# Performance work log

Hardware: AMD Instinct MI355X
Metric: run time of the kernel (lower is better)

The kernel has to match this reference:

```python
import jax, jax.numpy as jnp
import numpy as np

B, N, D = 8, 4096, 256

def setup_inputs() -> dict:
    key = jax.random.key(0)
    k1, k2, k3 = jax.random.split(key, 3)
    x = jax.random.normal(k1, (B, N, D), dtype=jnp.float32)
    # torch nn.Linear(D, 3D): weight [3D, D], bias [3D]
    W_qkv = jax.random.normal(k2, (3 * D, D), dtype=jnp.float32) * (1.0 / np.sqrt(D))
    b_qkv = jax.random.normal(k3, (3 * D,), dtype=jnp.float32) * 0.01
    return {"x": x, "W_qkv": W_qkv, "b_qkv": b_qkv}

def reference(x, W_qkv, b_qkv):
    Dm = x.shape[-1]
    qkv = jnp.einsum('bnd,ed->bne', x, W_qkv) + b_qkv  # [B,N,3D]
    q, k, v = jnp.split(qkv, 3, axis=-1)
    scale = 1.0 / jnp.sqrt(jnp.asarray(Dm, dtype=x.dtype))
    scores = jnp.einsum('bnd,bmd->bnm', q, k) * scale  # [B,N,N]
    attn = jax.nn.softmax(scores, axis=-1)
    return jnp.einsum('bnm,bmd->bnd', attn, v)
```

## Files before the change

### kernel.cpp

```cpp
#include <hip/hip_runtime.h>
#include <hip/hip_bf16.h>


typedef __attribute__((ext_vector_type(8))) short short8;
typedef __attribute__((ext_vector_type(4))) float f32x4;
typedef __attribute__((ext_vector_type(16))) float f32x16;

#define MFMA16(A, B, C) __builtin_amdgcn_mfma_f32_16x16x32_bf16(A, B, C, 0, 0, 0)
#define MFMA32(A, B, C) __builtin_amdgcn_mfma_f32_32x32x16_bf16(A, B, C, 0, 0, 0)

__device__ __forceinline__ unsigned short f2bf(float f) {
  union { float f; unsigned u; } v; v.f = f;
  unsigned r = v.u + 0x7FFFu + ((v.u >> 16) & 1u);
  return (unsigned short)(r >> 16);
}

__device__ __forceinline__ ushort4 pack4(float4 v) {
  ushort4 r;
  r.x = f2bf(v.x); r.y = f2bf(v.y); r.z = f2bf(v.z); r.w = f2bf(v.w);
  return r;
}

__device__ __forceinline__ unsigned packbf2(float a, float b) {
  union { __hip_bfloat162 b2; unsigned u; } cv;
  cv.b2 = __float22bfloat162_rn(make_float2(a, b));
  return cv.u;
}

__device__ __forceinline__ void gload_lds16(const void* g, void* l) {
  __builtin_amdgcn_global_load_lds(
      (const __attribute__((address_space(1))) void*)g,
      (__attribute__((address_space(3))) void*)l, 16, 0, 0);
}

template <int MODE>
__global__ __launch_bounds__(256)
void proj_kernel(const float* __restrict__ A, const float* __restrict__ Bm,
                 const float* __restrict__ bias,
                 unsigned short* __restrict__ Qs, unsigned short* __restrict__ Kb,
                 unsigned short* __restrict__ VT) {
  __shared__ __align__(16) unsigned short as_[2][128 * 64];
  __shared__ __align__(16) unsigned short bs_[2][128 * 64];

  const int tid = threadIdx.x;
  const int wid = tid >> 6, lane = tid & 63, l15 = lane & 15, lhi = lane >> 4;
  int m0, n0;
  if (MODE == 0) { m0 = blockIdx.y * 128; n0 = blockIdx.x * 128; }
  else           { m0 = blockIdx.x * 128; n0 = blockIdx.y * 128; }
  const float* Arow = A + (size_t)m0 * 256;
  const float* Brow = Bm + (size_t)n0 * 256;

  const int srow = tid >> 4;
  const int c4 = tid & 15;
  float4 ra[8], rb[8];

  auto loadslice = [&](int kc) {
#pragma unroll
    for (int i = 0; i < 8; ++i) {
      int row = i * 16 + srow;
      ra[i] = *(const float4*)(Arow + (size_t)row * 256 + kc * 64 + c4 * 4);
      rb[i] = *(const float4*)(Brow + (size_t)row * 256 + kc * 64 + c4 * 4);
    }
  };
  auto writeslice = [&](int buf) {
#pragma unroll
    for (int i = 0; i < 8; ++i) {
      int row = i * 16 + srow;
      int g = c4 >> 1, half = c4 & 1;
      int off = row * 64 + ((g ^ (row & 7)) << 3) + half * 4;
      *(ushort4*)&as_[buf][off] = pack4(ra[i]);
      *(ushort4*)&bs_[buf][off] = pack4(rb[i]);
    }
  };

  f32x4 acc[2][8];
#pragma unroll
  for (int mt = 0; mt < 2; ++mt)
#pragma unroll
    for (int nt = 0; nt < 8; ++nt) acc[mt][nt] = (f32x4){0.f, 0.f, 0.f, 0.f};

  loadslice(0);
  writeslice(0);
  int cur = 0;
  for (int kc = 0; kc < 4; ++kc) {
    __syncthreads();
    if (kc < 3) loadslice(kc + 1);
#pragma unroll
    for (int ks = 0; ks < 2; ++ks) {
      short8 af[2];
#pragma unroll
      for (int mt = 0; mt < 2; ++mt) {
        int row = wid * 32 + mt * 16 + l15;
        int g = ks * 4 + lhi;
        af[mt] = *(const short8*)&as_[cur][row * 64 + ((g ^ (row & 7)) << 3)];
      }
#pragma unroll
      for (int nt = 0; nt < 8; ++nt) {
        int row = nt * 16 + l15;
        int g = ks * 4 + lhi;
        short8 bf = *(const short8*)&bs_[cur][row * 64 + ((g ^ (row & 7)) << 3)];
        acc[0][nt] = MFMA16(af[0], bf, acc[0][nt]);
        acc[1][nt] = MFMA16(af[1], bf, acc[1][nt]);
      }
    }
    if (kc < 3) writeslice(cur ^ 1);
    cur ^= 1;
  }

  const float QSC = 0.0901684400555602f;
#pragma unroll
  for (int nt = 0; nt < 8; ++nt) {
    if (MODE == 0) {
      int e = n0 + nt * 16 + l15;
      float bv = bias[e];
#pragma unroll
      for (int mt = 0; mt < 2; ++mt)
#pragma unroll
        for (int r = 0; r < 4; ++r) {
          int tok = m0 + wid * 32 + mt * 16 + lhi * 4 + r;
          float val = acc[mt][nt][r] + bv;
          if (e < 256) Qs[(size_t)tok * 256 + e] = f2bf(val * QSC);
          else         Kb[(size_t)tok * 256 + (e - 256)] = f2bf(val);
        }
    } else {
      int tok = n0 + nt * 16 + l15;
      int bb = tok >> 12, n = tok & 4095;
      int t4 = n & 15;
      int flip = ((t4 >> 2) ^ (t4 >> 3)) & 1;
      int n2 = (n & ~15) | (t4 ^ (flip ? 12 : 0));
#pragma unroll
      for (int mt = 0; mt < 2; ++mt)
#pragma unroll
        for (int r = 0; r < 4; ++r) {
          int d = m0 + wid * 32 + mt * 16 + lhi * 4 + r;
          float val = acc[mt][nt][r] + bias[512 + d];
          VT[(size_t)bb * (256 * 4096) + (size_t)d * 4096 + n2] = f2bf(val);
        }
    }
  }
}

__global__ __launch_bounds__(256, 2)
void attn_split(const unsigned short* __restrict__ Qs,
                const unsigned short* __restrict__ Kb,
                const unsigned short* __restrict__ VT,
                float* __restrict__ out, float* __restrict__ O1,
                float2* __restrict__ ML) {
  __shared__ __align__(16) unsigned short lds_kv[2][16384];

  const int tid = threadIdx.x;
  const int wid = tid >> 6, lane = tid & 63, l31 = lane & 31, h = lane >> 5;
  const int blk = blockIdx.x;
  const int b = blk & 7;
  const int hh = (blk >> 3) & 1;
  const int qblk = blk >> 4;
  const int q0 = qblk * 128 + wid * 32;

  const unsigned short* qp = Qs + ((size_t)b * 4096 + q0 + l31) * 256 + h * 8;
  short8 qf[16];
#pragma unroll
  for (int ks = 0; ks < 16; ++ks) qf[ks] = *(const short8*)(qp + ks * 16);

  f32x16 acco[8];
#pragma unroll
  for (int dt = 0; dt < 8; ++dt)
#pragma unroll
    for (int j = 0; j < 16; ++j) acco[dt][j] = 0.f;
  float m = -1e30f, lsum = 0.f;

  const unsigned short* kbase = Kb + (size_t)b * 4096 * 256;
  const unsigned short* vtb   = VT + (size_t)b * 256 * 4096;

  auto stage = [&](int it, int buf) {
    const int kv0 = hh * 2048 + it * 32;
    unsigned short* kbuf = &lds_kv[buf][0];
    unsigned short* vbuf = &lds_kv[buf][8192];
    const unsigned short* ksrc = kbase + (size_t)kv0 * 256;
#pragma unroll
    for (int i = 0; i < 4; ++i) {
      int g = i * 256 + tid;
      int row = g >> 5, cp = g & 31;
      int sg = (row << 5) | (cp ^ (row & 7));
      gload_lds16(ksrc + sg * 8, kbuf + (i * 256 + (wid << 6)) * 8);
    }
#pragma unroll
    for (int i = 0; i < 4; ++i) {
      int g = i * 256 + tid;
      int d = g >> 2, cp = g & 3;
      int sc = cp ^ ((d >> 1) & 3);
      gload_lds16(vtb + (size_t)d * 4096 + kv0 + sc * 8,
                  vbuf + (i * 256 + (wid << 6)) * 8);
    }
  };

  stage(0, 0);
  int cur = 0;
  for (int it = 0; it < 64; ++it) {
    __syncthreads();
    if (it < 63) stage(it + 1, cur ^ 1);
    const unsigned short* kb = &lds_kv[cur][0];
    const unsigned short* vb = &lds_kv[cur][8192];

    f32x16 s0;
#pragma unroll
    for (int j = 0; j < 16; ++j) s0[j] = 0.f;
    __builtin_amdgcn_s_setprio(1);
#pragma unroll
    for (int ks = 0; ks < 16; ++ks) {
      const short8 kf =
          *(const short8*)&kb[l31 * 256 + (((2 * ks + h) ^ (l31 & 7)) << 3)];
      s0 = MFMA32(kf, qf[ks], s0);
    }
    __builtin_amdgcn_s_setprio(0);

    float mx = s0[0];
#pragma unroll
    for (int r = 1; r < 16; ++r) mx = fmaxf(mx, s0[r]);
    mx = fmaxf(mx, __shfl_xor(mx, 32));
    const float mo = m;
    const float mn = (mx > mo + 4.f) ? mx : mo;
    const float al = __builtin_amdgcn_exp2f(mo - mn);
    m = mn;
    if (__any(mn != mo)) {
      float alq[16];
#pragma unroll
      for (int r = 0; r < 16; ++r)
        alq[r] = __shfl(al, (r & 3) + 8 * (r >> 2) + 4 * h, 64);
#pragma unroll
      for (int dt = 0; dt < 8; ++dt)
#pragma unroll
        for (int r = 0; r < 16; ++r) acco[dt][r] *= alq[r];
    }

#pragma unroll
    for (int r = 0; r < 8; ++r) s0[r] = __builtin_amdgcn_exp2f(s0[r] - mn);
    short8 pf0;
    {
      union { unsigned u[4]; short8 v; } a0;
#pragma unroll
      for (int k2 = 0; k2 < 4; ++k2)
        a0.u[k2] = packbf2(s0[2 * k2], s0[2 * k2 + 1]);
      pf0 = a0.v;
    }
    __builtin_amdgcn_s_setprio(1);
#pragma unroll
    for (int dt = 0; dt < 8; ++dt) {
      const int d = dt * 32 + l31;
      const short8 vf =
          *(const short8*)&vb[d * 32 + ((h ^ ((l31 >> 1) & 3)) << 3)];
      acco[dt] = MFMA32(pf0, vf, acco[dt]);
    }
    __builtin_amdgcn_s_setprio(0);
#pragma unroll
    for (int r = 8; r < 16; ++r) s0[r] = __builtin_amdgcn_exp2f(s0[r] - mn);
    short8 pf1;
    {
      union { unsigned u[4]; short8 v; } a1;
#pragma unroll
      for (int k2 = 0; k2 < 4; ++k2)
        a1.u[k2] = packbf2(s0[8 + 2 * k2], s0[9 + 2 * k2]);
      pf1 = a1.v;
    }
    __builtin_amdgcn_s_setprio(1);
#pragma unroll
    for (int dt = 0; dt < 8; ++dt) {
      const int d = dt * 32 + l31;
      const short8 vf =
          *(const short8*)&vb[d * 32 + (((2 + h) ^ ((l31 >> 1) & 3)) << 3)];
      acco[dt] = MFMA32(pf1, vf, acco[dt]);
    }
    __builtin_amdgcn_s_setprio(0);

    float rs = 0.f;
#pragma unroll
    for (int r = 0; r < 16; ++r) rs += s0[r];
    rs += __shfl_xor(rs, 32);
    lsum = lsum * al + rs;
    cur ^= 1;
  }

  float* op = (hh ? O1 : out) + ((size_t)b * 4096 + q0) * 256;
#pragma unroll
  for (int dt = 0; dt < 8; ++dt)
#pragma unroll
    for (int r = 0; r < 16; ++r) {
      int qp2 = (r & 3) + 8 * (r >> 2) + 4 * h;
      op[(size_t)qp2 * 256 + dt * 32 + l31] = acco[dt][r];
    }
  if (lane < 32)
    ML[hh * 32768 + (size_t)b * 4096 + q0 + lane] = make_float2(m, lsum);
}

__global__ __launch_bounds__(256)
void merge_kernel(float* __restrict__ out, const float* __restrict__ O1,
                  const float2* __restrict__ ML) {
  const int i4 = blockIdx.x * 256 + threadIdx.x;
  const int row = i4 >> 6;
  const float2 s0 = ML[row], s1 = ML[32768 + row];
  const float mM = fmaxf(s0.x, s1.x);
  const float w0 = __builtin_amdgcn_exp2f(s0.x - mM);
  const float w1 = __builtin_amdgcn_exp2f(s1.x - mM);
  const float inv = 1.f / (w0 * s0.y + w1 * s1.y);
  const float4 a = ((const float4*)out)[i4];
  const float4 c = ((const float4*)O1)[i4];
  float4 r;
  r.x = (a.x * w0 + c.x * w1) * inv;
  r.y = (a.y * w0 + c.y * w1) * inv;
  r.z = (a.z * w0 + c.z * w1) * inv;
  r.w = (a.w * w0 + c.w * w1) * inv;
  ((float4*)out)[i4] = r;
}

__global__ __launch_bounds__(512, 2)
void attn_fused(const unsigned short* __restrict__ Qs,
                const unsigned short* __restrict__ Kb,
                const unsigned short* __restrict__ VT,
                float* __restrict__ out) {
  __shared__ __align__(16) unsigned short lds_kv[2][2][16384];
  __shared__ float2 lds_ml[8][32];

  const int tid = threadIdx.x;
  const int wid = tid >> 6, lane = tid & 63, l31 = lane & 31, h = lane >> 5;
  const int hv = wid >> 2;
  const int qg = wid & 3;
  const int tid_h = tid & 255;
  const int blk = blockIdx.x;
  const int b = blk & 7;
  const int qblk = blk >> 3;
  const int q0 = qblk * 128 + qg * 32;

  const unsigned short* qp = Qs + ((size_t)b * 4096 + q0 + l31) * 256 + h * 8;
  short8 qf[16];
#pragma unroll
  for (int ks = 0; ks < 16; ++ks) qf[ks] = *(const short8*)(qp + ks * 16);

  f32x16 acco[8];
#pragma unroll
  for (int dt = 0; dt < 8; ++dt)
#pragma unroll
    for (int j = 0; j < 16; ++j) acco[dt][j] = 0.f;
  float m = -1e30f, lsum = 0.f;

  const unsigned short* kbase = Kb + (size_t)b * 4096 * 256;
  const unsigned short* vtb   = VT + (size_t)b * 256 * 4096;

  auto stage = [&](int it, int buf) {
    const int kv0 = hv * 2048 + it * 32;
    unsigned short* kbuf = &lds_kv[hv][buf][0];
    unsigned short* vbuf = &lds_kv[hv][buf][8192];
    const unsigned short* ksrc = kbase + (size_t)kv0 * 256;
#pragma unroll
    for (int i = 0; i < 4; ++i) {
      int g = i * 256 + tid_h;
      int row = g >> 5, cp = g & 31;
      int sg = (row << 5) | (cp ^ (row & 7));
      gload_lds16(ksrc + sg * 8, kbuf + (i * 256 + (qg << 6)) * 8);
    }
#pragma unroll
    for (int i = 0; i < 4; ++i) {
      int g = i * 256 + tid_h;
      int d = g >> 2, cp = g & 3;
      int sc = cp ^ ((d >> 1) & 3);
      gload_lds16(vtb + (size_t)d * 4096 + kv0 + sc * 8,
                  vbuf + (i * 256 + (qg << 6)) * 8);
    }
  };

  stage(0, 0);
  int cur = 0;
  for (int it = 0; it < 64; ++it) {
    __syncthreads();
    if (it < 63) stage(it + 1, cur ^ 1);
    const unsigned short* kb = &lds_kv[hv][cur][0];
    const unsigned short* vb = &lds_kv[hv][cur][8192];

    f32x16 s0;
#pragma unroll
    for (int j = 0; j < 16; ++j) s0[j] = 0.f;
#pragma unroll
    for (int ks = 0; ks < 16; ++ks) {
      const short8 kf =
          *(const short8*)&kb[l31 * 256 + (((2 * ks + h) ^ (l31 & 7)) << 3)];
      s0 = MFMA32(kf, qf[ks], s0);
    }

    float mx = s0[0];
#pragma unroll
    for (int r = 1; r < 16; ++r) mx = fmaxf(mx, s0[r]);
    mx = fmaxf(mx, __shfl_xor(mx, 32));
    const float mo = m;
    const float mn = (mx > mo + 4.f) ? mx : mo;
    const float al = __builtin_amdgcn_exp2f(mo - mn);
    m = mn;
    if (__any(mn != mo)) {
      float alq[16];
#pragma unroll
      for (int r = 0; r < 16; ++r)
        alq[r] = __shfl(al, (r & 3) + 8 * (r >> 2) + 4 * h, 64);
#pragma unroll
      for (int dt = 0; dt < 8; ++dt)
#pragma unroll
        for (int r = 0; r < 16; ++r) acco[dt][r] *= alq[r];
    }

    float rs = 0.f;
#pragma unroll
    for (int r = 0; r < 16; ++r) {
      s0[r] = __builtin_amdgcn_exp2f(s0[r] - mn);
      rs += s0[r];
    }
    rs += __shfl_xor(rs, 32);
    lsum = lsum * al + rs;

    short8 pf[2];
    {
      union { unsigned u[4]; short8 v; } a0, a1;
#pragma unroll
      for (int k2 = 0; k2 < 4; ++k2) {
        a0.u[k2] = packbf2(s0[2 * k2], s0[2 * k2 + 1]);
        a1.u[k2] = packbf2(s0[8 + 2 * k2], s0[9 + 2 * k2]);
      }
      pf[0] = a0.v; pf[1] = a1.v;
    }
#pragma unroll
    for (int ks = 0; ks < 2; ++ks) {
#pragma unroll
      for (int dt = 0; dt < 8; ++dt) {
        const int d = dt * 32 + l31;
        const short8 vf = *(const short8*)
            &vb[d * 32 + (((2 * ks + h) ^ ((l31 >> 1) & 3)) << 3)];
        acco[dt] = MFMA32(pf[ks], vf, acco[dt]);
      }
    }
    cur ^= 1;
  }

  __syncthreads();
  if (lane < 32) lds_ml[wid][lane] = make_float2(m, lsum);
  float* o_base = (float*)&lds_kv[0][0][0];
  if (hv == 1) {
    float* o = o_base + qg * 8192;
#pragma unroll
    for (int dt = 0; dt < 8; ++dt)
#pragma unroll
      for (int r = 0; r < 16; ++r) {
        int qp2 = (r & 3) + 8 * (r >> 2) + 4 * h;
        o[qp2 * 256 + dt * 32 + l31] = acco[dt][r];
      }
  }
  __syncthreads();
  if (hv == 0) {
    float* o = o_base + qg * 8192;
    float* orow = out + ((size_t)b * 4096 + q0) * 256;
#pragma unroll
    for (int r = 0; r < 16; ++r) {
      int qp2 = (r & 3) + 8 * (r >> 2) + 4 * h;
      float2 s_own = lds_ml[wid][qp2];
      float2 s_par = lds_ml[wid + 4][qp2];
      float mM = fmaxf(s_own.x, s_par.x);
      float w0 = __builtin_amdgcn_exp2f(s_own.x - mM);
      float w1 = __builtin_amdgcn_exp2f(s_par.x - mM);
      float inv = 1.f / (w0 * s_own.y + w1 * s_par.y);
#pragma unroll
      for (int dt = 0; dt < 8; ++dt) {
        float val = (acco[dt][r] * w0 + o[qp2 * 256 + dt * 32 + l31] * w1) * inv;
        orow[(size_t)qp2 * 256 + dt * 32 + l31] = val;
      }
    }
  }
}

extern "C" void kernel_launch(void* const* d_in, const int* in_sizes, int n_in,
                              void* d_out, int out_size, void* d_ws, size_t ws_size,
                              hipStream_t stream) {
  const float* x    = (const float*)d_in[0];
  const float* W    = (const float*)d_in[1];
  const float* bias = (const float*)d_in[2];
  float* out = (float*)d_out;

  char* ws = (char*)d_ws;
  unsigned short* Qs = (unsigned short*)(ws);
  unsigned short* Kb = (unsigned short*)(ws + (size_t)16 * 1024 * 1024);
  unsigned short* VT = (unsigned short*)(ws + (size_t)32 * 1024 * 1024);
  float*          O1 = (float*)(ws + (size_t)48 * 1024 * 1024);
  float2*         ML = (float2*)(ws + (size_t)80 * 1024 * 1024);

  proj_kernel<0><<<dim3(4, 256), 256, 0, stream>>>(x, W, bias, Qs, Kb, VT);
  proj_kernel<1><<<dim3(2, 256), 256, 0, stream>>>(W + 512 * 256, x, bias, Qs, Kb, VT);

  const size_t NEED = (size_t)81 * 1024 * 1024;
  if (ws_size >= NEED) {
    attn_split<<<512, 256, 0, stream>>>(Qs, Kb, VT, out, O1, ML);
    merge_kernel<<<8192, 256, 0, stream>>>(out, O1, ML);
  } else {
    attn_fused<<<256, 512, 0, stream>>>(Qs, Kb, VT, out);
  }
}
```

Before: 243.7 us.

## Load K and V fragments directly from global memory instead of LDS staging

```diff
diff --git a/kernel.cpp b/kernel.cpp
--- a/kernel.cpp
+++ b/kernel.cpp
@@ -141,13 +141,11 @@
 }
 
 __global__ __launch_bounds__(256, 2)
-void attn_split(const unsigned short* __restrict__ Qs,
-                const unsigned short* __restrict__ Kb,
-                const unsigned short* __restrict__ VT,
-                float* __restrict__ out, float* __restrict__ O1,
-                float2* __restrict__ ML) {
-  __shared__ __align__(16) unsigned short lds_kv[2][16384];
-
+void attn_direct(const unsigned short* __restrict__ Qs,
+                 const unsigned short* __restrict__ Kb,
+                 const unsigned short* __restrict__ VT,
+                 float* __restrict__ out, float* __restrict__ O1,
+                 float2* __restrict__ ML) {
   const int tid = threadIdx.x;
   const int wid = tid >> 6, lane = tid & 63, l31 = lane & 31, h = lane >> 5;
   const int blk = blockIdx.x;
@@ -168,38 +166,12 @@
     for (int j = 0; j < 16; ++j) acco[dt][j] = 0.f;
   float m = -1e30f, lsum = 0.f;
 
-  const unsigned short* kbase = Kb + (size_t)b * 4096 * 256;
-  const unsigned short* vtb   = VT + (size_t)b * 256 * 4096;
-
-  auto stage = [&](int it, int buf) {
-    const int kv0 = hh * 2048 + it * 32;
-    unsigned short* kbuf = &lds_kv[buf][0];
-    unsigned short* vbuf = &lds_kv[buf][8192];
-    const unsigned short* ksrc = kbase + (size_t)kv0 * 256;
-#pragma unroll
-    for (int i = 0; i < 4; ++i) {
-      int g = i * 256 + tid;
-      int row = g >> 5, cp = g & 31;
-      int sg = (row << 5) | (cp ^ (row & 7));
-      gload_lds16(ksrc + sg * 8, kbuf + (i * 256 + (wid << 6)) * 8);
-    }
-#pragma unroll
-    for (int i = 0; i < 4; ++i) {
-      int g = i * 256 + tid;
-      int d = g >> 2, cp = g & 3;
-      int sc = cp ^ ((d >> 1) & 3);
-      gload_lds16(vtb + (size_t)d * 4096 + kv0 + sc * 8,
-                  vbuf + (i * 256 + (wid << 6)) * 8);
-    }
-  };
-
-  stage(0, 0);
-  int cur = 0;
+  const unsigned short* krow =
+      Kb + ((size_t)b * 4096 + hh * 2048 + l31) * 256 + h * 8;
+  const unsigned short* vrow = VT + (size_t)b * 256 * 4096 + hh * 2048;
+
   for (int it = 0; it < 64; ++it) {
-    __syncthreads();
-    if (it < 63) stage(it + 1, cur ^ 1);
-    const unsigned short* kb = &lds_kv[cur][0];
-    const unsigned short* vb = &lds_kv[cur][8192];
+    const int kv0 = it * 32;
 
     f32x16 s0;
 #pragma unroll
@@ -207,15 +179,17 @@
     __builtin_amdgcn_s_setprio(1);
 #pragma unroll
     for (int ks = 0; ks < 16; ++ks) {
-      const short8 kf =
-          *(const short8*)&kb[l31 * 256 + (((2 * ks + h) ^ (l31 & 7)) << 3)];
+      const short8 kf = *(const short8*)(krow + (size_t)kv0 * 256 + ks * 16);
       s0 = MFMA32(kf, qf[ks], s0);
     }
     __builtin_amdgcn_s_setprio(0);
 
-    float mx = s0[0];
-#pragma unroll
-    for (int r = 1; r < 16; ++r) mx = fmaxf(mx, s0[r]);
+    float m01 = fmaxf(s0[0], s0[1]),   m23 = fmaxf(s0[2], s0[3]);
+    float m45 = fmaxf(s0[4], s0[5]),   m67 = fmaxf(s0[6], s0[7]);
+    float m89 = fmaxf(s0[8], s0[9]),   mab = fmaxf(s0[10], s0[11]);
+    float mcd = fmaxf(s0[12], s0[13]), mef = fmaxf(s0[14], s0[15]);
+    float mx = fmaxf(fmaxf(fmaxf(m01, m23), fmaxf(m45, m67)),
+                     fmaxf(fmaxf(m89, mab), fmaxf(mcd, mef)));
     mx = fmaxf(mx, __shfl_xor(mx, 32));
     const float mo = m;
     const float mn = (mx > mo + 4.f) ? mx : mo;
@@ -247,7 +221,7 @@
     for (int dt = 0; dt < 8; ++dt) {
       const int d = dt * 32 + l31;
       const short8 vf =
-          *(const short8*)&vb[d * 32 + ((h ^ ((l31 >> 1) & 3)) << 3)];
+          *(const short8*)(vrow + (size_t)d * 4096 + kv0 + h * 8);
       acco[dt] = MFMA32(pf0, vf, acco[dt]);
     }
     __builtin_amdgcn_s_setprio(0);
@@ -266,7 +240,7 @@
     for (int dt = 0; dt < 8; ++dt) {
       const int d = dt * 32 + l31;
       const short8 vf =
-          *(const short8*)&vb[d * 32 + (((2 + h) ^ ((l31 >> 1) & 3)) << 3)];
+          *(const short8*)(vrow + (size_t)d * 4096 + kv0 + 16 + h * 8);
       acco[dt] = MFMA32(pf1, vf, acco[dt]);
     }
     __builtin_amdgcn_s_setprio(0);
@@ -276,7 +250,6 @@
     for (int r = 0; r < 16; ++r) rs += s0[r];
     rs += __shfl_xor(rs, 32);
     lsum = lsum * al + rs;
-    cur ^= 1;
   }
 
   float* op = (hh ? O1 : out) + ((size_t)b * 4096 + q0) * 256;
@@ -490,7 +463,7 @@
 
   const size_t NEED = (size_t)81 * 1024 * 1024;
   if (ws_size >= NEED) {
-    attn_split<<<512, 256, 0, stream>>>(Qs, Kb, VT, out, O1, ML);
+    attn_direct<<<512, 256, 0, stream>>>(Qs, Kb, VT, out, O1, ML);
     merge_kernel<<<8192, 256, 0, stream>>>(out, O1, ML);
   } else {
     attn_fused<<<256, 512, 0, stream>>>(Qs, Kb, VT, out);
```

Measured after the change: 546.8 us. +124.4%, slower.

## Fuse split-KV merge into attention kernel via last-block atomic ticket

Applied to the files above, without the earlier changes.

```diff
diff --git a/kernel.cpp b/kernel.cpp
--- a/kernel.cpp
+++ b/kernel.cpp
@@ -38,7 +38,10 @@
 void proj_kernel(const float* __restrict__ A, const float* __restrict__ Bm,
                  const float* __restrict__ bias,
                  unsigned short* __restrict__ Qs, unsigned short* __restrict__ Kb,
-                 unsigned short* __restrict__ VT) {
+                 unsigned short* __restrict__ VT, int* __restrict__ ticket) {
+  if (MODE == 0 && blockIdx.x == 0 && blockIdx.y == 0 && threadIdx.x < 256)
+    ticket[threadIdx.x] = 0;
+
   __shared__ __align__(16) unsigned short as_[2][128 * 64];
   __shared__ __align__(16) unsigned short bs_[2][128 * 64];
 
@@ -145,8 +148,9 @@
                 const unsigned short* __restrict__ Kb,
                 const unsigned short* __restrict__ VT,
                 float* __restrict__ out, float* __restrict__ O1,
-                float2* __restrict__ ML) {
+                float2* __restrict__ ML, int* __restrict__ ticket) {
   __shared__ __align__(16) unsigned short lds_kv[2][16384];
+  __shared__ int s_last;
 
   const int tid = threadIdx.x;
   const int wid = tid >> 6, lane = tid & 63, l31 = lane & 31, h = lane >> 5;
@@ -289,26 +293,39 @@
     }
   if (lane < 32)
     ML[hh * 32768 + (size_t)b * 4096 + q0 + lane] = make_float2(m, lsum);
-}
-
-__global__ __launch_bounds__(256)
-void merge_kernel(float* __restrict__ out, const float* __restrict__ O1,
-                  const float2* __restrict__ ML) {
-  const int i4 = blockIdx.x * 256 + threadIdx.x;
-  const int row = i4 >> 6;
-  const float2 s0 = ML[row], s1 = ML[32768 + row];
-  const float mM = fmaxf(s0.x, s1.x);
-  const float w0 = __builtin_amdgcn_exp2f(s0.x - mM);
-  const float w1 = __builtin_amdgcn_exp2f(s1.x - mM);
-  const float inv = 1.f / (w0 * s0.y + w1 * s1.y);
-  const float4 a = ((const float4*)out)[i4];
-  const float4 c = ((const float4*)O1)[i4];
-  float4 r;
-  r.x = (a.x * w0 + c.x * w1) * inv;
-  r.y = (a.y * w0 + c.y * w1) * inv;
-  r.z = (a.z * w0 + c.z * w1) * inv;
-  r.w = (a.w * w0 + c.w * w1) * inv;
-  ((float4*)out)[i4] = r;
+
+  __threadfence();
+  __syncthreads();
+  if (tid == 0) s_last = atomicAdd(&ticket[(b << 5) | qblk], 1);
+  __syncthreads();
+  if (s_last == 1) {
+    __threadfence();
+    float mq[16], lq[16];
+#pragma unroll
+    for (int r = 0; r < 16; ++r) {
+      int src = (r & 3) + 8 * (r >> 2) + 4 * h;
+      mq[r] = __shfl(m, src, 64);
+      lq[r] = __shfl(lsum, src, 64);
+    }
+    const float* pp = (hh ? out : O1) + ((size_t)b * 4096 + q0) * 256;
+    const float2* pml = ML + (hh ^ 1) * 32768 + (size_t)b * 4096 + q0;
+    float* orow = out + ((size_t)b * 4096 + q0) * 256;
+#pragma unroll
+    for (int r = 0; r < 16; ++r) {
+      int qp2 = (r & 3) + 8 * (r >> 2) + 4 * h;
+      float2 other = pml[qp2];
+      float mM = fmaxf(mq[r], other.x);
+      float w0 = __builtin_amdgcn_exp2f(mq[r] - mM);
+      float w1 = __builtin_amdgcn_exp2f(other.x - mM);
+      float inv = 1.f / (w0 * lq[r] + w1 * other.y);
+#pragma unroll
+      for (int dt = 0; dt < 8; ++dt) {
+        float val =
+            (acco[dt][r] * w0 + pp[(size_t)qp2 * 256 + dt * 32 + l31] * w1) * inv;
+        orow[(size_t)qp2 * 256 + dt * 32 + l31] = val;
+      }
+    }
+  }
 }
 
 __global__ __launch_bounds__(512, 2)
@@ -484,14 +501,14 @@
   unsigned short* VT = (unsigned short*)(ws + (size_t)32 * 1024 * 1024);
   float*          O1 = (float*)(ws + (size_t)48 * 1024 * 1024);
   float2*         ML = (float2*)(ws + (size_t)80 * 1024 * 1024);
-
-  proj_kernel<0><<<dim3(4, 256), 256, 0, stream>>>(x, W, bias, Qs, Kb, VT);
-  proj_kernel<1><<<dim3(2, 256), 256, 0, stream>>>(W + 512 * 256, x, bias, Qs, Kb, VT);
+  int*        ticket = (int*)(ws + (size_t)80 * 1024 * 1024 + 512 * 1024);
+
+  proj_kernel<0><<<dim3(4, 256), 256, 0, stream>>>(x, W, bias, Qs, Kb, VT, ticket);
+  proj_kernel<1><<<dim3(2, 256), 256, 0, stream>>>(W + 512 * 256, x, bias, Qs, Kb, VT, ticket);
 
   const size_t NEED = (size_t)81 * 1024 * 1024;
   if (ws_size >= NEED) {
-    attn_split<<<512, 256, 0, stream>>>(Qs, Kb, VT, out, O1, ML);
-    merge_kernel<<<8192, 256, 0, stream>>>(out, O1, ML);
+    attn_split<<<512, 256, 0, stream>>>(Qs, Kb, VT, out, O1, ML, ticket);
   } else {
     attn_fused<<<256, 512, 0, stream>>>(Qs, Kb, VT, out);
   }
```

New measurement: 364.8 us. 1.5x slower.
